# Kernel tuning notes

Measured on AMD Instinct MI355X. Metric: run time of the kernel, lower is better.

## Reference

```python
import jax, jax.numpy as jnp
import numpy as np

N_NODES = 50000
N_EDGES = 800000
IN_DIM = 768
HIDDEN = 256
N_CLASSES = 10
N_GRAPHS = 128


def setup_inputs() -> dict:
    key = jax.random.key(0)
    ks = jax.random.split(key, 10)
    emb = jax.random.normal(ks[0], (N_NODES, IN_DIM), dtype=jnp.float32)
    edge_index = jax.random.randint(ks[1], (2, N_EDGES), 0, N_NODES, dtype=jnp.int32)
    batch = jnp.sort(jax.random.randint(ks[2], (N_NODES,), 0, N_GRAPHS, dtype=jnp.int32))
    # GCNConv weights (glorot-ish scale) and biases
    W1 = jax.random.normal(ks[3], (IN_DIM, HIDDEN), dtype=jnp.float32) / np.sqrt(IN_DIM)
    b1 = jnp.zeros((HIDDEN,), dtype=jnp.float32)
    W2 = jax.random.normal(ks[4], (HIDDEN, HIDDEN), dtype=jnp.float32) / np.sqrt(HIDDEN)
    b2 = jnp.zeros((HIDDEN,), dtype=jnp.float32)
    Wfc = jax.random.normal(ks[5], (HIDDEN, N_CLASSES), dtype=jnp.float32) / np.sqrt(HIDDEN)
    bfc = jnp.zeros((N_CLASSES,), dtype=jnp.float32)
    return {"emb": emb, "edge_index": edge_index, "batch": batch,
            "W1": W1, "b1": b1, "W2": W2, "b2": b2, "Wfc": Wfc, "bfc": bfc}


def _gcn_conv(x, src, dst, W, b, n_nodes):
    # PyG GCNConv: x' = D^{-1/2} (A + I) D^{-1/2} X W + b, self-loops included
    h = x @ W                                   # [N, H] dense GEMM
    deg = jax.ops.segment_sum(jnp.ones_like(dst, dtype=h.dtype), dst,
                              num_segments=n_nodes)
    dinv = jnp.where(deg > 0, jax.lax.rsqrt(deg), 0.0)
    norm = dinv[src] * dinv[dst]                # [E+N]
    msgs = h[src] * norm[:, None]               # gather [E+N, H]
    out = jax.ops.segment_sum(msgs, dst, num_segments=n_nodes)  # scatter-add
    return out + b


def reference(emb, edge_index, batch, W1, b1, W2, b2, Wfc, bfc):
    n_nodes = emb.shape[0]
    loops = jnp.arange(n_nodes, dtype=edge_index.dtype)
    src = jnp.concatenate([edge_index[0], loops])  # add self-loops
    dst = jnp.concatenate([edge_index[1], loops])

    x = jax.nn.relu(_gcn_conv(emb, src, dst, W1, b1, n_nodes))
    # F.dropout(p=0.3) is a no-op in eval mode (training=False)
    x = _gcn_conv(x, src, dst, W2, b2, n_nodes)

    # global_mean_pool over graph ids
    sums = jax.ops.segment_sum(x, batch, num_segments=N_GRAPHS)
    cnts = jax.ops.segment_sum(jnp.ones((n_nodes,), dtype=x.dtype), batch,
                               num_segments=N_GRAPHS)
    pooled = sums / jnp.maximum(cnts, 1.0)[:, None]  # [G, H]
    return pooled @ Wfc + bfc                        # [G, C]
```

## Files before the change

### kernel.cpp

```cpp
#include <hip/hip_runtime.h>

#define N_NODES 50000
#define N_EDGES 800000
#define IN_DIM 768
#define HIDDEN 256
#define N_CLASSES 10
#define N_GRAPHS 128

typedef __attribute__((ext_vector_type(8))) short bf16x8;
typedef __attribute__((ext_vector_type(4))) float f32x4;

__device__ __forceinline__ float bf2f(unsigned short u) {
    union { unsigned int i; float f; } c; c.i = ((unsigned int)u) << 16; return c.f;
}
__device__ __forceinline__ unsigned short f2bf(float f) {
    unsigned int x = __float_as_uint(f);
    return (unsigned short)((x + 0x7fffu + ((x >> 16) & 1u)) >> 16);
}

__device__ __forceinline__ void gload16(const void* g, void* l) {
    __builtin_amdgcn_global_load_lds((const __attribute__((address_space(1))) void*)g,
                                     (__attribute__((address_space(3))) void*)l, 16, 0, 0);
}

__global__ void zero_int(int* p, int n) {
    int i = blockIdx.x * blockDim.x + threadIdx.x;
    if (i < n) p[i] = 0;
}

__global__ void zero_f32(float* p, int n) {
    int i = blockIdx.x * blockDim.x + threadIdx.x;
    if (i < n) p[i] = 0.f;
}

__global__ void hist_dst(const int* __restrict__ dst, int* __restrict__ cnt) {
    int e = blockIdx.x * blockDim.x + threadIdx.x;
    if (e < N_EDGES) atomicAdd(&cnt[dst[e]], 1);
}

__global__ void make_dinv(const int* __restrict__ cnt, float* __restrict__ dinv) {
    int i = blockIdx.x * blockDim.x + threadIdx.x;
    if (i < N_NODES) dinv[i] = rsqrtf(1.0f + (float)cnt[i]);
}

__global__ __launch_bounds__(1024) void scan_kernel(const int* __restrict__ cnt,
                                                    int* __restrict__ rowstart,
                                                    int* __restrict__ cursor) {
    __shared__ int wsum[16];
    __shared__ int chunk_carry;
    const int tid = threadIdx.x, lane = tid & 63, wid = tid >> 6;
    if (tid == 0) chunk_carry = 0;
    __syncthreads();
    for (int base = 0; base < N_NODES; base += 1024) {
        int i = base + tid;
        int v = (i < N_NODES) ? cnt[i] : 0;
        int s = v;
#pragma unroll
        for (int d = 1; d < 64; d <<= 1) { int t = __shfl_up(s, d); if (lane >= d) s += t; }
        if (lane == 63) wsum[wid] = s;
        __syncthreads();
        if (tid < 16) {
            int ww = wsum[tid];
#pragma unroll
            for (int d = 1; d < 16; d <<= 1) { int t = __shfl_up(ww, d); if (tid >= d) ww += t; }
            wsum[tid] = ww;
        }
        __syncthreads();
        int wpre = (wid == 0) ? 0 : wsum[wid - 1];
        int excl = chunk_carry + wpre + s - v;
        if (i < N_NODES) { rowstart[i] = excl; cursor[i] = excl; }
        int total = wsum[15];
        __syncthreads();
        if (tid == 0) chunk_carry += total;
        __syncthreads();
    }
    if (threadIdx.x == 0) rowstart[N_NODES] = chunk_carry;
}

__global__ void scatter_edges(const int* __restrict__ src, const int* __restrict__ dst,
                              int* __restrict__ cursor, int* __restrict__ col) {
    int e = blockIdx.x * blockDim.x + threadIdx.x;
    if (e >= N_EDGES) return;
    int d = dst[e];
    int pos = atomicAdd(&cursor[d], 1);
    col[pos] = src[e];
}

__global__ void f32_to_bf16(const float* __restrict__ in, unsigned short* __restrict__ out, int n8) {
    int i = blockIdx.x * blockDim.x + threadIdx.x;
    if (i >= n8) return;
    float4 v0 = *(const float4*)&in[(size_t)i * 8];
    float4 v1 = *(const float4*)&in[(size_t)i * 8 + 4];
    *(ushort4*)&out[(size_t)i * 8] =
        make_ushort4(f2bf(v0.x), f2bf(v0.y), f2bf(v0.z), f2bf(v0.w));
    *(ushort4*)&out[(size_t)i * 8 + 4] =
        make_ushort4(f2bf(v1.x), f2bf(v1.y), f2bf(v1.z), f2bf(v1.w));
}

__global__ void transpose_w_bf16(const float* __restrict__ W, unsigned short* __restrict__ WT, int K) {
    int k = blockIdx.x * 256 + threadIdx.x;
    int n = blockIdx.y;
    WT[(size_t)n * K + k] = f2bf(W[(size_t)k * 256 + n]);
}

template <int K>
__global__ __launch_bounds__(256) void gemm_mfma(const unsigned short* __restrict__ A,
                                                 const unsigned short* __restrict__ BT,
                                                 unsigned short* __restrict__ C, int M) {
    __shared__ uint4 sm[3072];
    uint4* As = sm;
    uint4* Bs = sm + 1024;
    const int tid = threadIdx.x;
    const int lane = tid & 63, w = tid >> 6;
    const int lr = lane & 15, kg = lane >> 4;
    const int bm = blockIdx.x * 128;

    f32x4 acc[2][16] = {};

    for (int k0 = 0; k0 < K; k0 += 64) {
#pragma unroll
        for (int i = 0; i < 4; ++i) {
            int glin = w * 256 + i * 64 + lane;
            int r = glin >> 3, g = glin & 7;
            int gs = g ^ (r & 7);
            int rg = bm + r; rg = rg < M ? rg : M - 1;
            gload16(&A[(size_t)rg * K + k0 + gs * 8], &As[w * 256 + i * 64]);
        }
#pragma unroll
        for (int i = 0; i < 8; ++i) {
            int glin = w * 512 + i * 64 + lane;
            int n = glin >> 3, g = glin & 7;
            int gs = g ^ (n & 7);
            gload16(&BT[(size_t)n * K + k0 + gs * 8], &Bs[w * 512 + i * 64]);
        }
        __syncthreads();

#pragma unroll
        for (int h = 0; h < 2; ++h) {
            int r0 = 32 * w + lr, r1 = r0 + 16;
            bf16x8 a0 = *(const bf16x8*)&As[r0 * 8 + ((4 * h + kg) ^ (r0 & 7))];
            bf16x8 a1 = *(const bf16x8*)&As[r1 * 8 + ((4 * h + kg) ^ (r1 & 7))];
#pragma unroll
            for (int f = 0; f < 16; ++f) {
                int nr = 16 * f + lr;
                bf16x8 bf = *(const bf16x8*)&Bs[nr * 8 + ((4 * h + kg) ^ (nr & 7))];
                acc[0][f] = __builtin_amdgcn_mfma_f32_16x16x32_bf16(bf, a0, acc[0][f], 0, 0, 0);
                acc[1][f] = __builtin_amdgcn_mfma_f32_16x16x32_bf16(bf, a1, acc[1][f], 0, 0, 0);
            }
        }
        __syncthreads();
    }
#pragma unroll
    for (int m = 0; m < 2; ++m) {
        int orow = bm + 32 * w + 16 * m + lr;
        if (orow < M) {
#pragma unroll
            for (int f = 0; f < 16; ++f) {
                ushort4 o = make_ushort4(f2bf(acc[m][f][0]), f2bf(acc[m][f][1]),
                                         f2bf(acc[m][f][2]), f2bf(acc[m][f][3]));
                *(ushort4*)&C[(size_t)orow * 256 + 16 * f + 4 * kg] = o;
            }
        }
    }
}

template <bool RELU, bool OUTBF>
__global__ __launch_bounds__(256) void agg_csr(const unsigned short* __restrict__ h,
                                               const float* __restrict__ dinv,
                                               const int* __restrict__ rowstart,
                                               const int* __restrict__ col,
                                               const float* __restrict__ bias,
                                               void* __restrict__ outv) {
    int node = (blockIdx.x * 256 + threadIdx.x) >> 6;
    if (node >= N_NODES) return;
    int lane = threadIdx.x & 63;

    float dd = dinv[node];
    float ww = dd * dd;
    ushort4 hv = *(const ushort4*)&h[(size_t)node * 256 + (lane << 2)];
    float a0 = bf2f(hv.x) * ww, a1 = bf2f(hv.y) * ww, a2 = bf2f(hv.z) * ww, a3 = bf2f(hv.w) * ww;

    int j = rowstart[node], jend = rowstart[node + 1];
    for (; j + 1 < jend; j += 2) {
        int sa = col[j], sb = col[j + 1];
        float na = dinv[sa] * dd, nb = dinv[sb] * dd;
        ushort4 va = *(const ushort4*)&h[(size_t)sa * 256 + (lane << 2)];
        ushort4 vb = *(const ushort4*)&h[(size_t)sb * 256 + (lane << 2)];
        a0 += bf2f(va.x) * na + bf2f(vb.x) * nb;
        a1 += bf2f(va.y) * na + bf2f(vb.y) * nb;
        a2 += bf2f(va.z) * na + bf2f(vb.z) * nb;
        a3 += bf2f(va.w) * na + bf2f(vb.w) * nb;
    }
    if (j < jend) {
        int sa = col[j];
        float na = dinv[sa] * dd;
        ushort4 va = *(const ushort4*)&h[(size_t)sa * 256 + (lane << 2)];
        a0 += bf2f(va.x) * na; a1 += bf2f(va.y) * na;
        a2 += bf2f(va.z) * na; a3 += bf2f(va.w) * na;
    }

    const float4 bb = *(const float4*)&bias[lane << 2];
    a0 += bb.x; a1 += bb.y; a2 += bb.z; a3 += bb.w;
    if (RELU) {
        a0 = fmaxf(a0, 0.f); a1 = fmaxf(a1, 0.f);
        a2 = fmaxf(a2, 0.f); a3 = fmaxf(a3, 0.f);
    }
    if (OUTBF) {
        *(ushort4*)((unsigned short*)outv + (size_t)node * 256 + (lane << 2)) =
            make_ushort4(f2bf(a0), f2bf(a1), f2bf(a2), f2bf(a3));
    } else {
        *(float4*)((float*)outv + (size_t)node * 256 + (lane << 2)) =
            make_float4(a0, a1, a2, a3);
    }
}

__global__ void graph_bounds(const int* __restrict__ batch, int* __restrict__ bounds) {
    int g = threadIdx.x;
    if (g < N_GRAPHS) {
        int lo = 0, hi = N_NODES;
        while (lo < hi) { int mid = (lo + hi) >> 1; if (batch[mid] < g) lo = mid + 1; else hi = mid; }
        bounds[g] = lo;
    }
    if (g == 0) bounds[N_GRAPHS] = N_NODES;
}

#define POOL_CHUNK 49
__global__ __launch_bounds__(256) void pool_partial(const float* __restrict__ x,
                                                    const int* __restrict__ batch,
                                                    float* __restrict__ gsum) {
    int lo = blockIdx.x * POOL_CHUNK;
    if (lo >= N_NODES) return;
    int hi = lo + POOL_CHUNK; if (hi > N_NODES) hi = N_NODES;
    int c = threadIdx.x;
    int g = batch[lo];
    float acc = 0.f;
    for (int n = lo; n < hi; ++n) {
        int gn = batch[n];
        if (gn != g) { atomicAdd(&gsum[g * 256 + c], acc); acc = 0.f; g = gn; }
        acc += x[(size_t)n * 256 + c];
    }
    atomicAdd(&gsum[g * 256 + c], acc);
}

__global__ __launch_bounds__(256) void fc_head(const float* __restrict__ gsum,
                                               const int* __restrict__ bounds,
                                               const float* __restrict__ Wfc,
                                               const float* __restrict__ bfc,
                                               float* __restrict__ out) {
    int g = blockIdx.x;
    int c = threadIdx.x;
    float inv = 1.0f / fmaxf((float)(bounds[g + 1] - bounds[g]), 1.0f);
    __shared__ float pooled[256];
    pooled[c] = gsum[(size_t)g * 256 + c] * inv;
    __syncthreads();
    if (c < N_CLASSES) {
        float acc = bfc[c];
        for (int k = 0; k < 256; ++k) acc += pooled[k] * Wfc[k * N_CLASSES + c];
        out[g * N_CLASSES + c] = acc;
    }
}

extern "C" void kernel_launch(void* const* d_in, const int* in_sizes, int n_in,
                              void* d_out, int out_size, void* d_ws, size_t ws_size,
                              hipStream_t stream) {
    const float* emb  = (const float*)d_in[0];
    const int*   eidx = (const int*)d_in[1];
    const int*   batch= (const int*)d_in[2];
    const float* W1   = (const float*)d_in[3];
    const float* b1   = (const float*)d_in[4];
    const float* W2   = (const float*)d_in[5];
    const float* b2   = (const float*)d_in[6];
    const float* Wfc  = (const float*)d_in[7];
    const float* bfc  = (const float*)d_in[8];
    float* out = (float*)d_out;

    const int* src = eidx;
    const int* dst = eidx + N_EDGES;

    char* ws = (char*)d_ws;
    size_t off = 0;
    auto alloc = [&](size_t bytes) { void* p = ws + off; off += (bytes + 1023) & ~(size_t)1023; return p; };
    int*   rowcnt   = (int*)alloc(N_NODES * 4);
    int*   rowstart = (int*)alloc((N_NODES + 1) * 4);
    int*   cursor   = (int*)alloc(N_NODES * 4);
    int*   col      = (int*)alloc(N_EDGES * 4);
    float* dinv     = (float*)alloc(N_NODES * 4);
    int*   bounds   = (int*)alloc((N_GRAPHS + 1) * 4);
    float* gsum     = (float*)alloc((size_t)N_GRAPHS * 256 * 4);
    unsigned short* W1T = (unsigned short*)alloc((size_t)HIDDEN * IN_DIM * 2);
    unsigned short* W2T = (unsigned short*)alloc((size_t)HIDDEN * HIDDEN * 2);
    unsigned short* bufH = (unsigned short*)alloc((size_t)N_NODES * 256 * 2);
    unsigned short* R = (unsigned short*)alloc((size_t)N_NODES * IN_DIM * 2);
    unsigned short* emb_bf = R;
    unsigned short* x1 = R;
    float* x2 = (float*)(R + (size_t)N_NODES * 256);

    const int NB = (N_NODES + 255) / 256;
    const int EBk = (N_EDGES + 255) / 256;
    const int AGG_B = (N_NODES * 64 + 255) / 256;
    dim3 gemm_grid((N_NODES + 127) / 128, 1);
    const int POOL_B = (N_NODES + POOL_CHUNK - 1) / POOL_CHUNK;

    zero_int<<<NB, 256, 0, stream>>>(rowcnt, N_NODES);
    hist_dst<<<EBk, 256, 0, stream>>>(dst, rowcnt);
    make_dinv<<<NB, 256, 0, stream>>>(rowcnt, dinv);
    scan_kernel<<<1, 1024, 0, stream>>>(rowcnt, rowstart, cursor);
    scatter_edges<<<EBk, 256, 0, stream>>>(src, dst, cursor, col);
    graph_bounds<<<1, 128, 0, stream>>>(batch, bounds);
    zero_f32<<<(N_GRAPHS * 256 + 255) / 256, 256, 0, stream>>>(gsum, N_GRAPHS * 256);

    f32_to_bf16<<<(N_NODES * IN_DIM / 8 + 255) / 256, 256, 0, stream>>>(emb, emb_bf, N_NODES * IN_DIM / 8);
    transpose_w_bf16<<<dim3(IN_DIM / 256, HIDDEN), 256, 0, stream>>>(W1, W1T, IN_DIM);
    transpose_w_bf16<<<dim3(HIDDEN / 256, HIDDEN), 256, 0, stream>>>(W2, W2T, HIDDEN);

    gemm_mfma<IN_DIM><<<gemm_grid, 256, 0, stream>>>(emb_bf, W1T, bufH, N_NODES);
    agg_csr<true, true><<<AGG_B, 256, 0, stream>>>(bufH, dinv, rowstart, col, b1, x1);

    gemm_mfma<HIDDEN><<<gemm_grid, 256, 0, stream>>>(x1, W2T, bufH, N_NODES);
    agg_csr<false, false><<<AGG_B, 256, 0, stream>>>(bufH, dinv, rowstart, col, b2, x2);

    pool_partial<<<POOL_B, 256, 0, stream>>>(x2, batch, gsum);
    fc_head<<<N_GRAPHS, 256, 0, stream>>>(gsum, bounds, Wfc, bfc, out);
}
```

Baseline: 458.6 us.

## Fuse input bf16 conversion into GEMM, widen aggregation loads, merge small kernels

```diff
diff --git a/kernel.cpp b/kernel.cpp
--- a/kernel.cpp
+++ b/kernel.cpp
@@ -9,6 +9,7 @@
 
 typedef __attribute__((ext_vector_type(8))) short bf16x8;
 typedef __attribute__((ext_vector_type(4))) float f32x4;
+typedef __attribute__((ext_vector_type(8))) unsigned short u16x8;
 
 __device__ __forceinline__ float bf2f(unsigned short u) {
     union { unsigned int i; float f; } c; c.i = ((unsigned int)u) << 16; return c.f;
@@ -38,14 +39,10 @@
     if (e < N_EDGES) atomicAdd(&cnt[dst[e]], 1);
 }
 
-__global__ void make_dinv(const int* __restrict__ cnt, float* __restrict__ dinv) {
-    int i = blockIdx.x * blockDim.x + threadIdx.x;
-    if (i < N_NODES) dinv[i] = rsqrtf(1.0f + (float)cnt[i]);
-}
-
 __global__ __launch_bounds__(1024) void scan_kernel(const int* __restrict__ cnt,
                                                     int* __restrict__ rowstart,
-                                                    int* __restrict__ cursor) {
+                                                    int* __restrict__ cursor,
+                                                    float* __restrict__ dinv) {
     __shared__ int wsum[16];
     __shared__ int chunk_carry;
     const int tid = threadIdx.x, lane = tid & 63, wid = tid >> 6;
@@ -54,6 +51,7 @@
     for (int base = 0; base < N_NODES; base += 1024) {
         int i = base + tid;
         int v = (i < N_NODES) ? cnt[i] : 0;
+        if (i < N_NODES) dinv[i] = rsqrtf(1.0f + (float)v);
         int s = v;
 #pragma unroll
         for (int d = 1; d < 64; d <<= 1) { int t = __shfl_up(s, d); if (lane >= d) s += t; }
@@ -86,25 +84,26 @@
     col[pos] = src[e];
 }
 
-__global__ void f32_to_bf16(const float* __restrict__ in, unsigned short* __restrict__ out, int n8) {
-    int i = blockIdx.x * blockDim.x + threadIdx.x;
-    if (i >= n8) return;
-    float4 v0 = *(const float4*)&in[(size_t)i * 8];
-    float4 v1 = *(const float4*)&in[(size_t)i * 8 + 4];
-    *(ushort4*)&out[(size_t)i * 8] =
-        make_ushort4(f2bf(v0.x), f2bf(v0.y), f2bf(v0.z), f2bf(v0.w));
-    *(ushort4*)&out[(size_t)i * 8 + 4] =
-        make_ushort4(f2bf(v1.x), f2bf(v1.y), f2bf(v1.z), f2bf(v1.w));
-}
-
-__global__ void transpose_w_bf16(const float* __restrict__ W, unsigned short* __restrict__ WT, int K) {
-    int k = blockIdx.x * 256 + threadIdx.x;
-    int n = blockIdx.y;
-    WT[(size_t)n * K + k] = f2bf(W[(size_t)k * 256 + n]);
-}
-
-template <int K>
-__global__ __launch_bounds__(256) void gemm_mfma(const unsigned short* __restrict__ A,
+__global__ __launch_bounds__(256) void transpose_w_bf16(const float* __restrict__ W,
+                                                        unsigned short* __restrict__ WT, int K) {
+    __shared__ float t[32][33];
+    int tx = threadIdx.x & 31, ty = threadIdx.x >> 5;
+    int k0 = blockIdx.x * 32, n0 = blockIdx.y * 32;
+#pragma unroll
+    for (int i = 0; i < 4; ++i) {
+        int k = k0 + ty + i * 8;
+        t[ty + i * 8][tx] = W[(size_t)k * 256 + n0 + tx];
+    }
+    __syncthreads();
+#pragma unroll
+    for (int i = 0; i < 4; ++i) {
+        int n = n0 + ty + i * 8;
+        WT[(size_t)n * K + k0 + tx] = f2bf(t[tx][ty + i * 8]);
+    }
+}
+
+template <int K, bool CVT>
+__global__ __launch_bounds__(256) void gemm_mfma(const void* __restrict__ Av,
                                                  const unsigned short* __restrict__ BT,
                                                  unsigned short* __restrict__ C, int M) {
     __shared__ uint4 sm[3072];
@@ -118,13 +117,31 @@
     f32x4 acc[2][16] = {};
 
     for (int k0 = 0; k0 < K; k0 += 64) {
-#pragma unroll
-        for (int i = 0; i < 4; ++i) {
-            int glin = w * 256 + i * 64 + lane;
-            int r = glin >> 3, g = glin & 7;
-            int gs = g ^ (r & 7);
-            int rg = bm + r; rg = rg < M ? rg : M - 1;
-            gload16(&A[(size_t)rg * K + k0 + gs * 8], &As[w * 256 + i * 64]);
+        if constexpr (CVT) {
+            const float* Af = (const float*)Av;
+#pragma unroll
+            for (int i = 0; i < 4; ++i) {
+                int glin = i * 256 + tid, r = glin >> 3, g = glin & 7;
+                int gs = g ^ (r & 7);
+                int rg = bm + r; rg = rg < M ? rg : M - 1;
+                const float* p = &Af[(size_t)rg * K + k0 + gs * 8];
+                float4 u = *(const float4*)p;
+                float4 v = *(const float4*)(p + 4);
+                u16x8 o;
+                o[0] = f2bf(u.x); o[1] = f2bf(u.y); o[2] = f2bf(u.z); o[3] = f2bf(u.w);
+                o[4] = f2bf(v.x); o[5] = f2bf(v.y); o[6] = f2bf(v.z); o[7] = f2bf(v.w);
+                *(u16x8*)&As[r * 8 + g] = o;
+            }
+        } else {
+            const unsigned short* Ab = (const unsigned short*)Av;
+#pragma unroll
+            for (int i = 0; i < 4; ++i) {
+                int glin = w * 256 + i * 64 + lane;
+                int r = glin >> 3, g = glin & 7;
+                int gs = g ^ (r & 7);
+                int rg = bm + r; rg = rg < M ? rg : M - 1;
+                gload16(&Ab[(size_t)rg * K + k0 + gs * 8], &As[w * 256 + i * 64]);
+            }
         }
 #pragma unroll
         for (int i = 0; i < 8; ++i) {
@@ -173,55 +190,53 @@
                                                void* __restrict__ outv) {
     int node = (blockIdx.x * 256 + threadIdx.x) >> 6;
     if (node >= N_NODES) return;
-    int lane = threadIdx.x & 63;
+    const int lane = threadIdx.x & 63;
+    const int half = lane >> 5, sl = lane & 31;
 
     float dd = dinv[node];
-    float ww = dd * dd;
-    ushort4 hv = *(const ushort4*)&h[(size_t)node * 256 + (lane << 2)];
-    float a0 = bf2f(hv.x) * ww, a1 = bf2f(hv.y) * ww, a2 = bf2f(hv.z) * ww, a3 = bf2f(hv.w) * ww;
-
-    int j = rowstart[node], jend = rowstart[node + 1];
-    for (; j + 1 < jend; j += 2) {
-        int sa = col[j], sb = col[j + 1];
-        float na = dinv[sa] * dd, nb = dinv[sb] * dd;
-        ushort4 va = *(const ushort4*)&h[(size_t)sa * 256 + (lane << 2)];
-        ushort4 vb = *(const ushort4*)&h[(size_t)sb * 256 + (lane << 2)];
-        a0 += bf2f(va.x) * na + bf2f(vb.x) * nb;
-        a1 += bf2f(va.y) * na + bf2f(vb.y) * nb;
-        a2 += bf2f(va.z) * na + bf2f(vb.z) * nb;
-        a3 += bf2f(va.w) * na + bf2f(vb.w) * nb;
-    }
-    if (j < jend) {
-        int sa = col[j];
-        float na = dinv[sa] * dd;
-        ushort4 va = *(const ushort4*)&h[(size_t)sa * 256 + (lane << 2)];
-        a0 += bf2f(va.x) * na; a1 += bf2f(va.y) * na;
-        a2 += bf2f(va.z) * na; a3 += bf2f(va.w) * na;
-    }
-
-    const float4 bb = *(const float4*)&bias[lane << 2];
-    a0 += bb.x; a1 += bb.y; a2 += bb.z; a3 += bb.w;
-    if (RELU) {
-        a0 = fmaxf(a0, 0.f); a1 = fmaxf(a1, 0.f);
-        a2 = fmaxf(a2, 0.f); a3 = fmaxf(a3, 0.f);
-    }
-    if (OUTBF) {
-        *(ushort4*)((unsigned short*)outv + (size_t)node * 256 + (lane << 2)) =
-            make_ushort4(f2bf(a0), f2bf(a1), f2bf(a2), f2bf(a3));
-    } else {
-        *(float4*)((float*)outv + (size_t)node * 256 + (lane << 2)) =
-            make_float4(a0, a1, a2, a3);
-    }
-}
-
-__global__ void graph_bounds(const int* __restrict__ batch, int* __restrict__ bounds) {
-    int g = threadIdx.x;
-    if (g < N_GRAPHS) {
-        int lo = 0, hi = N_NODES;
-        while (lo < hi) { int mid = (lo + hi) >> 1; if (batch[mid] < g) lo = mid + 1; else hi = mid; }
-        bounds[g] = lo;
-    }
-    if (g == 0) bounds[N_GRAPHS] = N_NODES;
+    float acc[8] = {};
+
+    {
+        u16x8 hv = *(const u16x8*)&h[(size_t)node * 256 + sl * 8];
+        float wgt = half ? 0.f : dd * dd;
+#pragma unroll
+        for (int i = 0; i < 8; ++i) acc[i] += bf2f(hv[i]) * wgt;
+    }
+
+    int j0 = rowstart[node], jend = rowstart[node + 1];
+    for (int j = j0; j < jend; j += 2) {
+        int sidx = j + half;
+        bool p = sidx < jend;
+        int s = p ? col[sidx] : node;
+        float nrm = p ? dinv[s] * dd : 0.f;
+        u16x8 v = *(const u16x8*)&h[(size_t)s * 256 + sl * 8];
+#pragma unroll
+        for (int i = 0; i < 8; ++i) acc[i] += bf2f(v[i]) * nrm;
+    }
+
+#pragma unroll
+    for (int i = 0; i < 8; ++i) acc[i] += __shfl_xor(acc[i], 32);
+
+    if (half == 0) {
+        float4 b0 = *(const float4*)&bias[sl * 8];
+        float4 b1 = *(const float4*)&bias[sl * 8 + 4];
+        acc[0] += b0.x; acc[1] += b0.y; acc[2] += b0.z; acc[3] += b0.w;
+        acc[4] += b1.x; acc[5] += b1.y; acc[6] += b1.z; acc[7] += b1.w;
+        if (RELU) {
+#pragma unroll
+            for (int i = 0; i < 8; ++i) acc[i] = fmaxf(acc[i], 0.f);
+        }
+        if (OUTBF) {
+            u16x8 o;
+#pragma unroll
+            for (int i = 0; i < 8; ++i) o[i] = f2bf(acc[i]);
+            *(u16x8*)((unsigned short*)outv + (size_t)node * 256 + sl * 8) = o;
+        } else {
+            float* ob = (float*)outv + (size_t)node * 256 + sl * 8;
+            *(float4*)ob = make_float4(acc[0], acc[1], acc[2], acc[3]);
+            *(float4*)(ob + 4) = make_float4(acc[4], acc[5], acc[6], acc[7]);
+        }
+    }
 }
 
 #define POOL_CHUNK 49
@@ -243,13 +258,17 @@
 }
 
 __global__ __launch_bounds__(256) void fc_head(const float* __restrict__ gsum,
-                                               const int* __restrict__ bounds,
+                                               const int* __restrict__ batch,
                                                const float* __restrict__ Wfc,
                                                const float* __restrict__ bfc,
                                                float* __restrict__ out) {
     int g = blockIdx.x;
     int c = threadIdx.x;
-    float inv = 1.0f / fmaxf((float)(bounds[g + 1] - bounds[g]), 1.0f);
+    int lo = 0, hi = N_NODES;
+    while (lo < hi) { int m = (lo + hi) >> 1; if (batch[m] < g) lo = m + 1; else hi = m; }
+    int lo2 = lo, hi2 = N_NODES;
+    while (lo2 < hi2) { int m = (lo2 + hi2) >> 1; if (batch[m] < g + 1) lo2 = m + 1; else hi2 = m; }
+    float inv = 1.0f / fmaxf((float)(lo2 - lo), 1.0f);
     __shared__ float pooled[256];
     pooled[c] = gsum[(size_t)g * 256 + c] * inv;
     __syncthreads();
@@ -285,15 +304,12 @@
     int*   cursor   = (int*)alloc(N_NODES * 4);
     int*   col      = (int*)alloc(N_EDGES * 4);
     float* dinv     = (float*)alloc(N_NODES * 4);
-    int*   bounds   = (int*)alloc((N_GRAPHS + 1) * 4);
     float* gsum     = (float*)alloc((size_t)N_GRAPHS * 256 * 4);
     unsigned short* W1T = (unsigned short*)alloc((size_t)HIDDEN * IN_DIM * 2);
     unsigned short* W2T = (unsigned short*)alloc((size_t)HIDDEN * HIDDEN * 2);
     unsigned short* bufH = (unsigned short*)alloc((size_t)N_NODES * 256 * 2);
-    unsigned short* R = (unsigned short*)alloc((size_t)N_NODES * IN_DIM * 2);
-    unsigned short* emb_bf = R;
-    unsigned short* x1 = R;
-    float* x2 = (float*)(R + (size_t)N_NODES * 256);
+    unsigned short* x1 = (unsigned short*)alloc((size_t)N_NODES * 256 * 2);
+    float* x2 = (float*)alloc((size_t)N_NODES * 256 * 4);
 
     const int NB = (N_NODES + 255) / 256;
     const int EBk = (N_EDGES + 255) / 256;
@@ -303,22 +319,19 @@
 
     zero_int<<<NB, 256, 0, stream>>>(rowcnt, N_NODES);
     hist_dst<<<EBk, 256, 0, stream>>>(dst, rowcnt);
-    make_dinv<<<NB, 256, 0, stream>>>(rowcnt, dinv);
-    scan_kernel<<<1, 1024, 0, stream>>>(rowcnt, rowstart, cursor);
+    scan_kernel<<<1, 1024, 0, stream>>>(rowcnt, rowstart, cursor, dinv);
     scatter_edges<<<EBk, 256, 0, stream>>>(src, dst, cursor, col);
-    graph_bounds<<<1, 128, 0, stream>>>(batch, bounds);
     zero_f32<<<(N_GRAPHS * 256 + 255) / 256, 256, 0, stream>>>(gsum, N_GRAPHS * 256);
 
-    f32_to_bf16<<<(N_NODES * IN_DIM / 8 + 255) / 256, 256, 0, stream>>>(emb, emb_bf, N_NODES * IN_DIM / 8);
-    transpose_w_bf16<<<dim3(IN_DIM / 256, HIDDEN), 256, 0, stream>>>(W1, W1T, IN_DIM);
-    transpose_w_bf16<<<dim3(HIDDEN / 256, HIDDEN), 256, 0, stream>>>(W2, W2T, HIDDEN);
-
-    gemm_mfma<IN_DIM><<<gemm_grid, 256, 0, stream>>>(emb_bf, W1T, bufH, N_NODES);
+    transpose_w_bf16<<<dim3(IN_DIM / 32, 8), 256, 0, stream>>>(W1, W1T, IN_DIM);
+    transpose_w_bf16<<<dim3(HIDDEN / 32, 8), 256, 0, stream>>>(W2, W2T, HIDDEN);
+
+    gemm_mfma<IN_DIM, true><<<gemm_grid, 256, 0, stream>>>(emb, W1T, bufH, N_NODES);
     agg_csr<true, true><<<AGG_B, 256, 0, stream>>>(bufH, dinv, rowstart, col, b1, x1);
 
-    gemm_mfma<HIDDEN><<<gemm_grid, 256, 0, stream>>>(x1, W2T, bufH, N_NODES);
+    gemm_mfma<HIDDEN, false><<<gemm_grid, 256, 0, stream>>>(x1, W2T, bufH, N_NODES);
     agg_csr<false, false><<<AGG_B, 256, 0, stream>>>(bufH, dinv, rowstart, col, b2, x2);
 
     pool_partial<<<POOL_B, 256, 0, stream>>>(x2, batch, gsum);
-    fc_head<<<N_GRAPHS, 256, 0, stream>>>(gsum, bounds, Wfc, bfc, out);
-}
+    fc_head<<<N_GRAPHS, 256, 0, stream>>>(gsum, batch, Wfc, bfc, out);
+}
```

Result: no change. 450.1 us (-1.9%).
